# Kernel optimization log

Hardware: AMD Instinct MI355X
Metric: run time of the kernel (lower is better)

Reference implementation:

```python
import jax, jax.numpy as jnp
import numpy as np

N = 20000
E = 160000
H = 4      # heads
C = 128    # per-head out channels (hidden_dim)
HID = 128


def setup_inputs() -> dict:
    key = jax.random.key(0)
    ks = jax.random.split(key, 24)
    inp = {}
    inp["x"] = jax.random.normal(ks[0], (8,), jnp.float32)
    inp["des"] = jax.random.normal(ks[1], (N, 768), jnp.float32)
    inp["tweet"] = jax.random.normal(ks[2], (N, 768), jnp.float32)
    inp["num_prop"] = jax.random.normal(ks[3], (N, 5), jnp.float32)
    inp["cat_prop"] = jax.random.normal(ks[4], (N, 1), jnp.float32)
    inp["edge_index"] = jax.random.randint(ks[5], (2, E), 0, N, dtype=jnp.int64)
    inp["target_node_idx"] = 123
    s = lambda fan_in: 1.0 / np.sqrt(fan_in)
    u = lambda k, shp, b: jax.random.uniform(k, shp, jnp.float32, -b, b)
    inp["W_des"] = u(ks[6], (768, 32), s(768)); inp["b_des"] = u(ks[7], (32,), s(768))
    inp["W_tw"] = u(ks[8], (768, 32), s(768)); inp["b_tw"] = u(ks[9], (32,), s(768))
    inp["W_np"] = u(ks[10], (5, 32), s(5));   inp["b_np"] = u(ks[11], (32,), s(5))
    inp["W_cp"] = u(ks[12], (1, 32), s(1));   inp["b_cp"] = u(ks[13], (32,), s(1))
    inp["W_gat"] = u(ks[14], (HID, H * C), s(HID))      # GATConv lin (no bias)
    inp["att_src"] = u(ks[15], (H, C), s(C))
    inp["att_dst"] = u(ks[16], (H, C), s(C))
    inp["b_gat"] = jnp.zeros((C,), jnp.float32)
    inp["W_o1"] = u(ks[17], (HID + 8, 64), s(HID + 8)); inp["b_o1"] = u(ks[18], (64,), s(HID + 8))
    inp["W_o2"] = u(ks[19], (64, 5), s(64));            inp["b_o2"] = u(ks[20], (5,), s(64))
    return inp


def _gat_conv(feature, edge_index, W_gat, att_src, att_dst, b_gat):
    # add self-loops (PyG default)
    loops = jnp.arange(N, dtype=edge_index.dtype)
    src = jnp.concatenate([edge_index[0], loops])
    dst = jnp.concatenate([edge_index[1], loops])
    h = (feature @ W_gat).reshape(N, H, C)                 # [N,H,C]
    a_src = jnp.einsum("nhc,hc->nh", h, att_src)           # [N,H]
    a_dst = jnp.einsum("nhc,hc->nh", h, att_dst)
    e = jax.nn.leaky_relu(a_src[src] + a_dst[dst], 0.2)    # [E+N,H]
    m = jax.ops.segment_max(e, dst, num_segments=N)        # segment softmax (stable)
    ex = jnp.exp(e - m[dst])
    denom = jax.ops.segment_sum(ex, dst, num_segments=N)
    alpha = ex / denom[dst]                                # [E+N,H]
    out = jax.ops.segment_sum(alpha[:, :, None] * h[src], dst, num_segments=N)  # [N,H,C]
    return out.mean(axis=1) + b_gat                        # concat=False -> mean heads


def reference(x, des, tweet, num_prop, cat_prop, edge_index, target_node_idx,
              W_des, b_des, W_tw, b_tw, W_np, b_np, W_cp, b_cp,
              W_gat, att_src, att_dst, b_gat, W_o1, b_o1, W_o2, b_o2):
    lrelu = jax.nn.leaky_relu  # slope 0.01 (nn.LeakyReLU default)
    d = lrelu(des @ W_des + b_des)
    t = lrelu(tweet @ W_tw + b_tw)
    n = lrelu(num_prop @ W_np + b_np)
    c = lrelu(cat_prop @ W_cp + b_cp)
    feature = jnp.concatenate([d, t, n, c], axis=1)        # [N,128]
    gat_out = _gat_conv(feature, edge_index, W_gat, att_src, att_dst, b_gat)
    target_feat = gat_out[target_node_idx]                 # [128]
    combined = jnp.concatenate([target_feat, x], axis=0)   # [136]
    hmid = jax.nn.relu(combined @ W_o1 + b_o1)
    return hmid @ W_o2 + b_o2                              # [5]
```

## Files before the change

### kernel.cpp

```cpp
#include <hip/hip_runtime.h>
#include <math.h>

#define HEADS 4
#define CDIM 128
#define HDIM 512
#define FEAT 128
#define NBS 128
#define NT 512
#define REG 8
#define TGT_SID (NBS * REG)
#define NMAX 64

__global__ __launch_bounds__(NT)
void scan_process_kernel(const float* __restrict__ des, const float* __restrict__ tw,
                         const float* __restrict__ npr, const float* __restrict__ cpr,
                         const float* __restrict__ Wd, const float* __restrict__ bd,
                         const float* __restrict__ Wt, const float* __restrict__ bt,
                         const float* __restrict__ Wn, const float* __restrict__ bn,
                         const float* __restrict__ Wc, const float* __restrict__ bc,
                         const float* __restrict__ Wg, const float* __restrict__ Wo1,
                         const float* __restrict__ att_src, const float* __restrict__ att_dst,
                         const int* __restrict__ ei, int E,
                         const int* __restrict__ tgt_p,
                         int* __restrict__ blockCounts,
                         float* __restrict__ aS, float* __restrict__ aD,
                         float* __restrict__ h_all) {
    __shared__ float sdes[768];
    __shared__ float stw[768];
    __shared__ float snp8[8];
    __shared__ float sfeat[FEAT];
    __shared__ float part[NT];
    __shared__ float pr[2 * HDIM];
    __shared__ int   lmatch[REG];
    __shared__ int   lcount;

    const int tid = threadIdx.x;
    const int b = blockIdx.x;
    const int tgt = *tgt_p;
    const int wv = tid >> 6, lane = tid & 63;

    float keep = 0.f;
    {
        const int g = b * NT + tid;
        if (g < 6144)       { float4 v = ((const float4*)Wd)[g];           keep = v.x + v.y + v.z + v.w; }
        else if (g < 12288) { float4 v = ((const float4*)Wt)[g - 6144];    keep = v.x + v.y + v.z + v.w; }
        else if (g < 28672) { float4 v = ((const float4*)Wg)[g - 12288];   keep = v.x + v.y + v.z + v.w; }
        else if (g < 30848) { float4 v = ((const float4*)Wo1)[g - 28672];  keep = v.x + v.y + v.z + v.w; }
    }

    if (tid == 0) lcount = 0;
    __syncthreads();
    const int nquad = E >> 2;
    const int qb = (nquad + NBS - 1) / NBS;
    const int q0 = b * qb;
    const int qe = (q0 + qb < nquad) ? (q0 + qb) : nquad;
    for (int q = q0 + tid; q < qe; q += NT) {
        const int4 dd = *(const int4*)(ei + (size_t)E + (size_t)q * 4);
        const int base = q * 4;
        if (dd.x == tgt) { int p = atomicAdd(&lcount, 1); if (p < REG) lmatch[p] = ei[base + 0]; }
        if (dd.y == tgt) { int p = atomicAdd(&lcount, 1); if (p < REG) lmatch[p] = ei[base + 1]; }
        if (dd.z == tgt) { int p = atomicAdd(&lcount, 1); if (p < REG) lmatch[p] = ei[base + 2]; }
        if (dd.w == tgt) { int p = atomicAdd(&lcount, 1); if (p < REG) lmatch[p] = ei[base + 3]; }
    }
    if (b == NBS - 1) {
        for (int k = nquad * 4 + tid; k < E; k += NT)
            if (ei[E + k] == tgt) { int p = atomicAdd(&lcount, 1); if (p < REG) lmatch[p] = ei[k]; }
    }
    asm volatile("" :: "v"(keep));
    __syncthreads();

    const int mycount = (lcount < REG) ? lcount : REG;
    if (tid == 0) blockCounts[b] = mycount;

    const int nwork = mycount + ((b == 0) ? 1 : 0);
    for (int it = 0; it < nwork; ++it) {
        const bool isTgt = (b == 0) && (it == mycount);
        const int node = isTgt ? tgt : lmatch[it];
        const int sid  = isTgt ? TGT_SID : (b * REG + it);

        if (tid < 192) {
            ((float4*)sdes)[tid] = ((const float4*)(des + (size_t)node * 768))[tid];
            ((float4*)stw)[tid]  = ((const float4*)(tw  + (size_t)node * 768))[tid];
        } else if (tid < 197) {
            snp8[tid - 192] = npr[node * 5 + (tid - 192)];
        } else if (tid == 197) {
            snp8[5] = cpr[node];
        }
        __syncthreads();

        {
            const int half = tid >> 8;
            const int t2 = tid & 255;
            const int j = t2 & 31, ch = t2 >> 5;
            const float* W = half ? Wt : Wd;
            const float* S = half ? stw : sdes;
            const float* wp = W + (size_t)(ch * 96) * 32 + j;
            const float* sp = S + ch * 96;
            float p = 0.f;
            #pragma unroll 16
            for (int k = 0; k < 96; ++k) p = fmaf(sp[k], wp[(size_t)k * 32], p);
            part[tid] = p;
        }
        __syncthreads();
        if (tid < 32) {
            float a = bd[tid];
            #pragma unroll
            for (int c2 = 0; c2 < 8; ++c2) a += part[c2 * 32 + tid];
            sfeat[tid] = a > 0.f ? a : 0.01f * a;
        } else if (tid < 64) {
            const int jj = tid - 32;
            float a = bt[jj];
            #pragma unroll
            for (int c2 = 0; c2 < 8; ++c2) a += part[256 + c2 * 32 + jj];
            sfeat[32 + jj] = a > 0.f ? a : 0.01f * a;
        } else if (tid < 96) {
            const int jj = tid - 64;
            float a = bn[jj];
            #pragma unroll
            for (int k = 0; k < 5; ++k) a = fmaf(snp8[k], Wn[k * 32 + jj], a);
            sfeat[64 + jj] = a > 0.f ? a : 0.01f * a;
        } else if (tid < 128) {
            const int jj = tid - 96;
            float a = fmaf(snp8[5], Wc[jj], bc[jj]);
            sfeat[96 + jj] = a > 0.f ? a : 0.01f * a;
        }
        __syncthreads();

        {
            const float* wg = Wg + tid;
            float hv = 0.f;
            #pragma unroll 16
            for (int k = 0; k < FEAT; ++k) hv = fmaf(sfeat[k], wg[(size_t)k * HDIM], hv);
            h_all[(size_t)sid * HDIM + tid] = hv;
            pr[tid] = hv * att_src[tid];
            if (isTgt) pr[HDIM + tid] = hv * att_dst[tid];
        }
        __syncthreads();

        if (wv < 4) {
            float v = pr[wv * 128 + lane] + pr[wv * 128 + 64 + lane];
            #pragma unroll
            for (int off = 32; off > 0; off >>= 1) v += __shfl_down(v, off);
            if (lane == 0) aS[sid * HEADS + wv] = v;
        } else if (isTgt) {
            const int hd = wv - 4;
            float v = pr[HDIM + hd * 128 + lane] + pr[HDIM + hd * 128 + 64 + lane];
            #pragma unroll
            for (int off = 32; off > 0; off >>= 1) v += __shfl_down(v, off);
            if (lane == 0) aD[hd] = v;
        }
        __syncthreads();
    }
}

__global__ __launch_bounds__(NT)
void finalize_kernel(const float* __restrict__ x, const float* __restrict__ bgat,
                     const float* __restrict__ Wo1, const float* __restrict__ bo1,
                     const float* __restrict__ Wo2, const float* __restrict__ bo2,
                     const int* __restrict__ blockCounts,
                     const float* __restrict__ aS, const float* __restrict__ aD,
                     const float* __restrict__ h_all,
                     float* __restrict__ out) {
    __shared__ int   bc[NBS];
    __shared__ int   pf[NBS];
    __shared__ int   slots[NMAX];
    __shared__ float saS[NMAX * HEADS];
    __shared__ float saD[HEADS];
    __shared__ float pr[HDIM];
    __shared__ float scomb[144];
    __shared__ float shmid[64];
    __shared__ int   sM;

    const int tid = threadIdx.x;

    if (tid < NBS) { bc[tid] = blockCounts[tid]; pf[tid] = bc[tid]; }
    __syncthreads();
    for (int off = 1; off < NBS; off <<= 1) {
        int add = (tid < NBS && tid >= off) ? pf[tid - off] : 0;
        __syncthreads();
        if (tid < NBS) pf[tid] += add;
        __syncthreads();
    }
    if (tid < NBS) {
        const int excl = pf[tid] - bc[tid];
        for (int i = 0; i < bc[tid]; ++i) {
            const int p = excl + i;
            if (p < NMAX - 1) slots[p] = tid * REG + i;
        }
    }
    if (tid == 0) {
        int total = pf[NBS - 1];
        if (total > NMAX - 1) total = NMAX - 1;
        slots[total] = TGT_SID;
        sM = total + 1;
    }
    __syncthreads();
    const int M = sM;

    for (int i = tid; i < M * HEADS; i += NT) {
        const int s = i >> 2, hd = i & 3;
        saS[i] = aS[slots[s] * HEADS + hd];
    }
    if (tid < HEADS) saD[tid] = aD[tid];
    __syncthreads();

    {
        const int o = tid, hd = o >> 7;
        const float adv = saD[hd];
        float m = -INFINITY;
        for (int s = 0; s < M; ++s) {
            float e = saS[s * HEADS + hd] + adv;
            e = e > 0.f ? e : 0.2f * e;
            m = fmaxf(m, e);
        }
        float denom = 0.f, acc = 0.f;
        for (int s = 0; s < M; ++s) {
            float e = saS[s * HEADS + hd] + adv;
            e = e > 0.f ? e : 0.2f * e;
            const float ex = expf(e - m);
            denom += ex;
            acc = fmaf(ex, h_all[(size_t)slots[s] * HDIM + o], acc);
        }
        pr[o] = acc / denom;
    }
    __syncthreads();

    if (tid < 128) {
        scomb[tid] = (pr[tid] + pr[128 + tid] + pr[256 + tid] + pr[384 + tid]) * 0.25f
                     + bgat[tid];
    } else if (tid < 136) {
        scomb[tid] = x[tid - 128];
    }
    __syncthreads();

    if (tid < 64) {
        float a = bo1[tid];
        #pragma unroll 8
        for (int k = 0; k < 136; ++k) a = fmaf(scomb[k], Wo1[k * 64 + tid], a);
        shmid[tid] = a > 0.f ? a : 0.f;
    }
    __syncthreads();
    if (tid < 5) {
        float a = bo2[tid];
        #pragma unroll 8
        for (int k = 0; k < 64; ++k) a = fmaf(shmid[k], Wo2[k * 5 + tid], a);
        out[tid] = a;
    }
}

extern "C" void kernel_launch(void* const* d_in, const int* in_sizes, int n_in,
                              void* d_out, int out_size, void* d_ws, size_t ws_size,
                              hipStream_t stream) {
    const float* x    = (const float*)d_in[0];
    const float* des  = (const float*)d_in[1];
    const float* tw   = (const float*)d_in[2];
    const float* npr  = (const float*)d_in[3];
    const float* cpr  = (const float*)d_in[4];
    const int*   ei   = (const int*)d_in[5];
    const int*   tgt  = (const int*)d_in[6];
    const float* Wd   = (const float*)d_in[7];   const float* bd  = (const float*)d_in[8];
    const float* Wt   = (const float*)d_in[9];   const float* bt  = (const float*)d_in[10];
    const float* Wn   = (const float*)d_in[11];  const float* bn  = (const float*)d_in[12];
    const float* Wc   = (const float*)d_in[13];  const float* bc  = (const float*)d_in[14];
    const float* Wg   = (const float*)d_in[15];
    const float* as_  = (const float*)d_in[16];  const float* ad_ = (const float*)d_in[17];
    const float* bg   = (const float*)d_in[18];
    const float* Wo1  = (const float*)d_in[19];  const float* bo1 = (const float*)d_in[20];
    const float* Wo2  = (const float*)d_in[21];  const float* bo2 = (const float*)d_in[22];

    const int E = in_sizes[5] / 2;

    char* ws = (char*)d_ws;
    int*   blockCounts = (int*)ws;
    float* aS    = (float*)(ws + 1024);
    float* aD    = aS + (size_t)(TGT_SID + 1) * HEADS;
    float* h_all = aD + 16;

    scan_process_kernel<<<NBS, NT, 0, stream>>>(des, tw, npr, cpr,
                                                Wd, bd, Wt, bt, Wn, bn, Wc, bc,
                                                Wg, Wo1, as_, ad_,
                                                ei, E, tgt,
                                                blockCounts, aS, aD, h_all);

    finalize_kernel<<<1, NT, 0, stream>>>(x, bg, Wo1, bo1, Wo2, bo2,
                                          blockCounts, aS, aD, h_all, (float*)d_out);
}
```

Before: 19.72 us.

## Fuse scan and finalize kernels via last-block atomic counter

Merges the scan/process kernel and the single-block finalize kernel into one launch. The last block to finish, detected with an atomic counter after a threadfence, runs the finalize logic. Target-node processing moves to a dedicated extra block so block 0 no longer does double work. A tiny zero kernel resets the counter, so there are still two launches, and the change adds atomic and fence overhead plus higher shared-memory use per block.

```diff
diff --git a/kernel.cpp b/kernel.cpp
--- a/kernel.cpp
+++ b/kernel.cpp
@@ -11,20 +11,28 @@
 #define TGT_SID (NBS * REG)
 #define NMAX 64
 
+__global__ void zero_kernel(int* __restrict__ p) {
+    if (threadIdx.x == 0) p[0] = 0;
+}
+
 __global__ __launch_bounds__(NT)
-void scan_process_kernel(const float* __restrict__ des, const float* __restrict__ tw,
-                         const float* __restrict__ npr, const float* __restrict__ cpr,
-                         const float* __restrict__ Wd, const float* __restrict__ bd,
-                         const float* __restrict__ Wt, const float* __restrict__ bt,
-                         const float* __restrict__ Wn, const float* __restrict__ bn,
-                         const float* __restrict__ Wc, const float* __restrict__ bc,
-                         const float* __restrict__ Wg, const float* __restrict__ Wo1,
-                         const float* __restrict__ att_src, const float* __restrict__ att_dst,
-                         const int* __restrict__ ei, int E,
-                         const int* __restrict__ tgt_p,
-                         int* __restrict__ blockCounts,
-                         float* __restrict__ aS, float* __restrict__ aD,
-                         float* __restrict__ h_all) {
+void mega_kernel(const float* __restrict__ des, const float* __restrict__ tw,
+                 const float* __restrict__ npr, const float* __restrict__ cpr,
+                 const float* __restrict__ Wd, const float* __restrict__ bd,
+                 const float* __restrict__ Wt, const float* __restrict__ bt,
+                 const float* __restrict__ Wn, const float* __restrict__ bn,
+                 const float* __restrict__ Wc, const float* __restrict__ bc,
+                 const float* __restrict__ Wg,
+                 const float* __restrict__ att_src, const float* __restrict__ att_dst,
+                 const float* __restrict__ x, const float* __restrict__ bgat,
+                 const float* __restrict__ Wo1, const float* __restrict__ bo1,
+                 const float* __restrict__ Wo2, const float* __restrict__ bo2,
+                 const int* __restrict__ ei, int E,
+                 const int* __restrict__ tgt_p,
+                 int* __restrict__ done, int* __restrict__ blockCounts,
+                 float* __restrict__ aS, float* __restrict__ aD,
+                 float* __restrict__ h_all,
+                 float* __restrict__ out) {
     __shared__ float sdes[768];
     __shared__ float stw[768];
     __shared__ float snp8[8];
@@ -33,51 +41,22 @@
     __shared__ float pr[2 * HDIM];
     __shared__ int   lmatch[REG];
     __shared__ int   lcount;
+    __shared__ int   sIsLast;
+    __shared__ int   sbc[NBS];
+    __shared__ int   pf[NBS];
+    __shared__ int   slots[NMAX];
+    __shared__ float saS[NMAX * HEADS];
+    __shared__ float saD[HEADS];
+    __shared__ float scomb[144];
+    __shared__ float shmid[64];
+    __shared__ int   sM;
 
     const int tid = threadIdx.x;
     const int b = blockIdx.x;
     const int tgt = *tgt_p;
     const int wv = tid >> 6, lane = tid & 63;
 
-    float keep = 0.f;
-    {
-        const int g = b * NT + tid;
-        if (g < 6144)       { float4 v = ((const float4*)Wd)[g];           keep = v.x + v.y + v.z + v.w; }
-        else if (g < 12288) { float4 v = ((const float4*)Wt)[g - 6144];    keep = v.x + v.y + v.z + v.w; }
-        else if (g < 28672) { float4 v = ((const float4*)Wg)[g - 12288];   keep = v.x + v.y + v.z + v.w; }
-        else if (g < 30848) { float4 v = ((const float4*)Wo1)[g - 28672];  keep = v.x + v.y + v.z + v.w; }
-    }
-
-    if (tid == 0) lcount = 0;
-    __syncthreads();
-    const int nquad = E >> 2;
-    const int qb = (nquad + NBS - 1) / NBS;
-    const int q0 = b * qb;
-    const int qe = (q0 + qb < nquad) ? (q0 + qb) : nquad;
-    for (int q = q0 + tid; q < qe; q += NT) {
-        const int4 dd = *(const int4*)(ei + (size_t)E + (size_t)q * 4);
-        const int base = q * 4;
-        if (dd.x == tgt) { int p = atomicAdd(&lcount, 1); if (p < REG) lmatch[p] = ei[base + 0]; }
-        if (dd.y == tgt) { int p = atomicAdd(&lcount, 1); if (p < REG) lmatch[p] = ei[base + 1]; }
-        if (dd.z == tgt) { int p = atomicAdd(&lcount, 1); if (p < REG) lmatch[p] = ei[base + 2]; }
-        if (dd.w == tgt) { int p = atomicAdd(&lcount, 1); if (p < REG) lmatch[p] = ei[base + 3]; }
-    }
-    if (b == NBS - 1) {
-        for (int k = nquad * 4 + tid; k < E; k += NT)
-            if (ei[E + k] == tgt) { int p = atomicAdd(&lcount, 1); if (p < REG) lmatch[p] = ei[k]; }
-    }
-    asm volatile("" :: "v"(keep));
-    __syncthreads();
-
-    const int mycount = (lcount < REG) ? lcount : REG;
-    if (tid == 0) blockCounts[b] = mycount;
-
-    const int nwork = mycount + ((b == 0) ? 1 : 0);
-    for (int it = 0; it < nwork; ++it) {
-        const bool isTgt = (b == 0) && (it == mycount);
-        const int node = isTgt ? tgt : lmatch[it];
-        const int sid  = isTgt ? TGT_SID : (b * REG + it);
-
+    auto process_node = [&](int node, int sid, bool isTgt) {
         if (tid < 192) {
             ((float4*)sdes)[tid] = ((const float4*)(des + (size_t)node * 768))[tid];
             ((float4*)stw)[tid]  = ((const float4*)(tw  + (size_t)node * 768))[tid];
@@ -150,30 +129,60 @@
             if (lane == 0) aD[hd] = v;
         }
         __syncthreads();
-    }
-}
-
-__global__ __launch_bounds__(NT)
-void finalize_kernel(const float* __restrict__ x, const float* __restrict__ bgat,
-                     const float* __restrict__ Wo1, const float* __restrict__ bo1,
-                     const float* __restrict__ Wo2, const float* __restrict__ bo2,
-                     const int* __restrict__ blockCounts,
-                     const float* __restrict__ aS, const float* __restrict__ aD,
-                     const float* __restrict__ h_all,
-                     float* __restrict__ out) {
-    __shared__ int   bc[NBS];
-    __shared__ int   pf[NBS];
-    __shared__ int   slots[NMAX];
-    __shared__ float saS[NMAX * HEADS];
-    __shared__ float saD[HEADS];
-    __shared__ float pr[HDIM];
-    __shared__ float scomb[144];
-    __shared__ float shmid[64];
-    __shared__ int   sM;
-
-    const int tid = threadIdx.x;
-
-    if (tid < NBS) { bc[tid] = blockCounts[tid]; pf[tid] = bc[tid]; }
+    };
+
+    if (b < NBS) {
+        float keep = 0.f;
+        {
+            const int g = b * NT + tid;
+            if (g < 6144)       { float4 v = ((const float4*)Wd)[g];           keep = v.x + v.y + v.z + v.w; }
+            else if (g < 12288) { float4 v = ((const float4*)Wt)[g - 6144];    keep = v.x + v.y + v.z + v.w; }
+            else if (g < 28672) { float4 v = ((const float4*)Wg)[g - 12288];   keep = v.x + v.y + v.z + v.w; }
+            else if (g < 30848) { float4 v = ((const float4*)Wo1)[g - 28672];  keep = v.x + v.y + v.z + v.w; }
+        }
+
+        if (tid == 0) lcount = 0;
+        __syncthreads();
+        const int nquad = E >> 2;
+        const int qb = (nquad + NBS - 1) / NBS;
+        const int q0 = b * qb;
+        const int qe = (q0 + qb < nquad) ? (q0 + qb) : nquad;
+        for (int q = q0 + tid; q < qe; q += NT) {
+            const int4 dd = *(const int4*)(ei + (size_t)E + (size_t)q * 4);
+            const int base = q * 4;
+            if (dd.x == tgt) { int p = atomicAdd(&lcount, 1); if (p < REG) lmatch[p] = ei[base + 0]; }
+            if (dd.y == tgt) { int p = atomicAdd(&lcount, 1); if (p < REG) lmatch[p] = ei[base + 1]; }
+            if (dd.z == tgt) { int p = atomicAdd(&lcount, 1); if (p < REG) lmatch[p] = ei[base + 2]; }
+            if (dd.w == tgt) { int p = atomicAdd(&lcount, 1); if (p < REG) lmatch[p] = ei[base + 3]; }
+        }
+        if (b == NBS - 1) {
+            for (int k = nquad * 4 + tid; k < E; k += NT)
+                if (ei[E + k] == tgt) { int p = atomicAdd(&lcount, 1); if (p < REG) lmatch[p] = ei[k]; }
+        }
+        asm volatile("" :: "v"(keep));
+        __syncthreads();
+
+        const int mycount = (lcount < REG) ? lcount : REG;
+        if (tid == 0) blockCounts[b] = mycount;
+
+        for (int it = 0; it < mycount; ++it)
+            process_node(lmatch[it], b * REG + it, false);
+    } else {
+        process_node(tgt, TGT_SID, true);
+    }
+
+    __syncthreads();
+    if (tid == 0) {
+        __threadfence();
+        const int old = atomicAdd(done, 1);
+        const int last = (old == NBS);
+        if (last) __threadfence();
+        sIsLast = last;
+    }
+    __syncthreads();
+    if (!sIsLast) return;
+
+    if (tid < NBS) { sbc[tid] = blockCounts[tid]; pf[tid] = sbc[tid]; }
     __syncthreads();
     for (int off = 1; off < NBS; off <<= 1) {
         int add = (tid < NBS && tid >= off) ? pf[tid - off] : 0;
@@ -182,8 +191,8 @@
         __syncthreads();
     }
     if (tid < NBS) {
-        const int excl = pf[tid] - bc[tid];
-        for (int i = 0; i < bc[tid]; ++i) {
+        const int excl = pf[tid] - sbc[tid];
+        for (int i = 0; i < sbc[tid]; ++i) {
             const int p = excl + i;
             if (p < NMAX - 1) slots[p] = tid * REG + i;
         }
@@ -271,17 +280,19 @@
     const int E = in_sizes[5] / 2;
 
     char* ws = (char*)d_ws;
-    int*   blockCounts = (int*)ws;
+    int*   done        = (int*)ws;
+    int*   blockCounts = (int*)(ws + 256);
     float* aS    = (float*)(ws + 1024);
     float* aD    = aS + (size_t)(TGT_SID + 1) * HEADS;
     float* h_all = aD + 16;
 
-    scan_process_kernel<<<NBS, NT, 0, stream>>>(des, tw, npr, cpr,
-                                                Wd, bd, Wt, bt, Wn, bn, Wc, bc,
-                                                Wg, Wo1, as_, ad_,
-                                                ei, E, tgt,
-                                                blockCounts, aS, aD, h_all);
-
-    finalize_kernel<<<1, NT, 0, stream>>>(x, bg, Wo1, bo1, Wo2, bo2,
-                                          blockCounts, aS, aD, h_all, (float*)d_out);
+    zero_kernel<<<1, 64, 0, stream>>>(done);
+
+    mega_kernel<<<NBS + 1, NT, 0, stream>>>(des, tw, npr, cpr,
+                                            Wd, bd, Wt, bt, Wn, bn, Wc, bc,
+                                            Wg, as_, ad_,
+                                            x, bg, Wo1, bo1, Wo2, bo2,
+                                            ei, E, tgt,
+                                            done, blockCounts, aS, aD, h_all,
+                                            (float*)d_out);
 }
```

New measurement: 26.04 us. 1.32x slower.
